# Optimization experiments

Measured on AMD Instinct MI355X. Metric: run time of the kernel, lower is better.

The kernel has to match this reference:

```python
import jax, jax.numpy as jnp
import numpy as np

VSIZE = 100000
LENGTH = 200
BATCH = 1024

def setup_inputs() -> dict:
    key = jax.random.key(0)
    k1, k2, k3 = jax.random.split(key, 3)
    x = jax.random.randint(k1, (LENGTH, BATCH), 0, VSIZE, dtype=jnp.int64)
    # nn.Linear(vsize, 1): weight (1, vsize), bias (1,)
    bound = 1.0 / np.sqrt(VSIZE)
    W = jax.random.uniform(k2, (1, VSIZE), minval=-bound, maxval=bound, dtype=jnp.float32)
    b_lut = jax.random.uniform(k3, (1,), minval=-bound, maxval=bound, dtype=jnp.float32)
    bias = jnp.zeros((1,), dtype=jnp.float32)
    return {"x": x, "W": W, "b_lut": b_lut, "bias": bias}

def reference(x, W, b_lut, bias):
    # x: (length, batch) int token ids.
    # Original builds a (vsize, batch) presence indicator ((counts > 0).float())
    # then applies Linear(vsize, 1). Equivalent: presence[b, v] = 1 if token v
    # appears in column b, out[b] = presence[b] . W[0] + b_lut + bias.
    length, batch = x.shape
    bi = jnp.broadcast_to(jnp.arange(batch), (length, batch))
    presence = jnp.zeros((batch, VSIZE), dtype=jnp.float32).at[bi, x].set(1.0)
    out = presence @ W[0] + b_lut[0] + bias[0]  # (batch,)
    return out
```

## Files before the change

### kernel.cpp

```cpp
#include <hip/hip_runtime.h>


#define VSIZE     100000
#define LENGTH    200
#define BATCH     1024
#define HASH_SIZE 1024
#define EMPTY     0xFFFFFFFFu

__global__ __launch_bounds__(256) void LR2_kernel(
    const int* __restrict__ x,
    const float* __restrict__ W,
    const float* __restrict__ b_lut,
    const float* __restrict__ bias,
    float* __restrict__ out)
{
    __shared__ unsigned ht[HASH_SIZE];
    __shared__ float    wsum[4];

    const int b = blockIdx.x;
    const int t = threadIdx.x;

    unsigned tok = EMPTY;
    if (t < LENGTH) tok = (unsigned)x[t * BATCH + b];

    #pragma unroll
    for (int i = t; i < HASH_SIZE; i += 256) ht[i] = EMPTY;
    __syncthreads();

    float contrib = 0.0f;
    if (t < LENGTH) {
        unsigned h = (tok * 2654435761u) >> 22;
        for (;;) {
            unsigned old = atomicCAS(&ht[h], EMPTY, tok);
            if (old == EMPTY) {
                contrib = W[tok];
                break;
            }
            if (old == tok) break;
            h = (h + 1) & (HASH_SIZE - 1);
        }
    }

    for (int off = 32; off > 0; off >>= 1)
        contrib += __shfl_down(contrib, off, 64);

    const int wave = t >> 6;
    const int lane = t & 63;
    if (lane == 0) wsum[wave] = contrib;
    __syncthreads();

    if (t == 0) {
        float s = wsum[0] + wsum[1] + wsum[2] + wsum[3];
        out[b] = s + b_lut[0] + bias[0];
    }
}

extern "C" void kernel_launch(void* const* d_in, const int* in_sizes, int n_in,
                              void* d_out, int out_size, void* d_ws, size_t ws_size,
                              hipStream_t stream) {
    const int*   x     = (const int*)d_in[0];
    const float* W     = (const float*)d_in[1];
    const float* b_lut = (const float*)d_in[2];
    const float* bias  = (const float*)d_in[3];
    float*       out   = (float*)d_out;

    LR2_kernel<<<BATCH, 256, 0, stream>>>(x, W, b_lut, bias, out);
}
```

Measured before the change: 9.738 us.

## Process 16 batch columns per block with per-column shared hash tables

Each block now handles 16 batch columns instead of one. Each thread loads up to 13 tokens, with 16 consecutive threads reading contiguous columns so the loads coalesce, and dedups them serially into a per-column 512-entry shared hash table. This removes the strided one-column-per-block loads and the per-block overhead of 1024 blocks. The cost is only 64 blocks (low occupancy on a large GPU) and serial hash probing inside each thread, which adds latency.

```diff
diff --git a/kernel.cpp b/kernel.cpp
--- a/kernel.cpp
+++ b/kernel.cpp
@@ -1,11 +1,13 @@
 #include <hip/hip_runtime.h>
 
 
-#define VSIZE     100000
-#define LENGTH    200
-#define BATCH     1024
-#define HASH_SIZE 1024
-#define EMPTY     0xFFFFFFFFu
+#define VSIZE   100000
+#define LENGTH  200
+#define BATCH   1024
+#define COLS    16
+#define HBITS   9
+#define HSIZE   (1 << HBITS)
+#define EMPTY   0xFFFFFFFFu
 
 __global__ __launch_bounds__(256) void LR2_kernel(
     const int* __restrict__ x,
@@ -14,44 +16,50 @@
     const float* __restrict__ bias,
     float* __restrict__ out)
 {
-    __shared__ unsigned ht[HASH_SIZE];
-    __shared__ float    wsum[4];
+    __shared__ unsigned ht[COLS][HSIZE];
+    __shared__ float    partial[4][COLS];
 
-    const int b = blockIdx.x;
-    const int t = threadIdx.x;
+    const int t   = threadIdx.x;
+    const int col = t & (COLS - 1);
+    const int rg  = t >> 4;
+    const int c   = blockIdx.x * COLS + col;
 
-    unsigned tok = EMPTY;
-    if (t < LENGTH) tok = (unsigned)x[t * BATCH + b];
+    const int nrows = (rg < (LENGTH & (COLS - 1))) ? (LENGTH / COLS + 1)
+                                                   : (LENGTH / COLS);
 
+    unsigned toks[13];
     #pragma unroll
-    for (int i = t; i < HASH_SIZE; i += 256) ht[i] = EMPTY;
+    for (int k = 0; k < 13; ++k)
+        if (k < nrows)
+            toks[k] = (unsigned)x[(rg + COLS * k) * BATCH + c];
+
+    uint4* htv = (uint4*)&ht[0][0];
+    #pragma unroll
+    for (int i = t; i < COLS * HSIZE / 4; i += 256)
+        htv[i] = make_uint4(EMPTY, EMPTY, EMPTY, EMPTY);
     __syncthreads();
 
     float contrib = 0.0f;
-    if (t < LENGTH) {
-        unsigned h = (tok * 2654435761u) >> 22;
+    for (int k = 0; k < nrows; ++k) {
+        unsigned tok = toks[k];
+        unsigned h = (tok * 2654435761u) >> (32 - HBITS);
         for (;;) {
-            unsigned old = atomicCAS(&ht[h], EMPTY, tok);
-            if (old == EMPTY) {
-                contrib = W[tok];
-                break;
-            }
+            unsigned old = atomicCAS(&ht[col][h], EMPTY, tok);
+            if (old == EMPTY) { contrib += W[tok]; break; }
             if (old == tok) break;
-            h = (h + 1) & (HASH_SIZE - 1);
+            h = (h + 1) & (HSIZE - 1);
         }
     }
 
-    for (int off = 32; off > 0; off >>= 1)
-        contrib += __shfl_down(contrib, off, 64);
-
+    contrib += __shfl_xor(contrib, 16, 64);
+    contrib += __shfl_xor(contrib, 32, 64);
     const int wave = t >> 6;
-    const int lane = t & 63;
-    if (lane == 0) wsum[wave] = contrib;
+    if ((t & 63) < COLS) partial[wave][col] = contrib;
     __syncthreads();
 
-    if (t == 0) {
-        float s = wsum[0] + wsum[1] + wsum[2] + wsum[3];
-        out[b] = s + b_lut[0] + bias[0];
+    if (t < COLS) {
+        float s = partial[0][t] + partial[1][t] + partial[2][t] + partial[3][t];
+        out[blockIdx.x * COLS + t] = s + b_lut[0] + bias[0];
     }
 }
 
@@ -64,5 +72,5 @@
     const float* bias  = (const float*)d_in[3];
     float*       out   = (float*)d_out;
 
-    LR2_kernel<<<BATCH, 256, 0, stream>>>(x, W, b_lut, bias, out);
+    LR2_kernel<<<BATCH / COLS, 256, 0, stream>>>(x, W, b_lut, bias, out);
 }
```

New measurement: 19.68 us. 102% more time.
